# Kernel optimization log

Measured on AMD Instinct MI355X. Metric: run time of the kernel, lower is better.

## Reference

```python
import jax, jax.numpy as jnp
import numpy as np

B, F0, D = 2048, 39, 16
LAYER_SIZES = [128, 128, 128]  # split_half=True -> field_nums [39, 64, 64]


def setup_inputs() -> dict:
    key = jax.random.key(0)
    ks = jax.random.split(key, 1 + 2 * len(LAYER_SIZES))
    inputs = jax.random.normal(ks[0], (B, F0, D), dtype=jnp.float32)
    out = {"inputs": inputs}
    field_nums = [F0]
    for i, size in enumerate(LAYER_SIZES):
        fk = field_nums[-1]
        fan_in = F0 * fk  # conv1d filter fan-in (kernel width 1)
        scale = np.sqrt(2.0 / (fan_in + size)).astype(np.float32)  # glorot
        # filter stored as [F0, Fk, size]; TF flat index is h0*Fk + hk
        out[f"w{i}"] = jax.random.normal(ks[1 + 2 * i], (F0, fk, size), dtype=jnp.float32) * scale
        out[f"b{i}"] = jnp.zeros((size,), dtype=jnp.float32)
        field_nums.append(size // 2)  # split_half=True
    return out


def reference(inputs, w0, w1, w2, b0, b1, b2):
    # CIN: per-embedding-dim outer product of x0 and x_{k-1}, then 1x1 conv
    # (shared dense over field pairs). Fused here as a single einsum per layer.
    x0 = inputs  # [B, F0, D]
    xk = inputs  # [B, Fk, D]
    params = [(w0, b0), (w1, b1), (w2, b2)]
    n_layers = len(params)
    direct = []
    for idx, (W, b) in enumerate(params):
        # out[b, s, d] = sum_{h,k} x0[b,h,d] * xk[b,k,d] * W[h,k,s]
        z = jnp.einsum('bhd,bkd,hks->bsd', x0, xk, W) + b[None, :, None]
        z = jax.nn.relu(z)  # activation='relu'
        if idx != n_layers - 1:
            half = z.shape[1] // 2  # split_half: first half feeds next layer
            xk = z[:, :half, :]
            direct.append(z[:, half:, :])
        else:
            direct.append(z)
    logit = jnp.sum(jnp.concatenate(direct, axis=1), axis=-1)  # [B, 64+64+128]
    return logit
```

## Files before the change

### kernel.cpp

```cpp
#include <hip/hip_runtime.h>
#include <stdint.h>
#include <stddef.h>

#define F0N  39
#define SN   128
#define NB   4
#define X0TS 44
#define XKTS 72
#define WBLK 8192
#define NHB  117

typedef __attribute__((ext_vector_type(8))) short short8;
typedef __attribute__((ext_vector_type(4))) float floatx4;

__device__ __forceinline__ uint16_t f2bf(float f) {
  uint32_t u = __float_as_uint(f);
  u += 0x7fffu + ((u >> 16) & 1u);
  return (uint16_t)(u >> 16);
}

__global__ __launch_bounds__(256) void cin_prepass(
    const float* __restrict__ w0, const float* __restrict__ w1,
    const float* __restrict__ w2, uint16_t* __restrict__ wt) {
  __shared__ float T[64 * 132];
  const int bc = blockIdx.x;
  const int L = bc / F0N;
  const int h = bc - L * F0N;
  const float* W = (L == 0) ? w0 : ((L == 1) ? w1 : w2);
  const int fk = (L == 0) ? 39 : 64;
  const int tid = threadIdx.x;

  for (int e = tid; e < 8192; e += 256) {
    int k = e >> 7, s = e & 127;
    T[k * 132 + s] = (k < fk) ? W[(h * fk + k) * SN + s] : 0.0f;
  }
  __syncthreads();
  uint32_t* dst = (uint32_t*)(wt + (size_t)bc * WBLK);
  for (int i = tid; i < 4096; i += 256) {
    int frag = i >> 8, w = i & 255;
    int st = frag >> 1, ch = frag & 1;
    int ln = w >> 2, jp = w & 3;
    int quad = ln >> 4, l16 = ln & 15;
    int k0 = ch * 32 + quad * 8 + jp * 2;
    int s = st * 16 + l16;
    dst[i] = (uint32_t)f2bf(T[k0 * 132 + s]) | ((uint32_t)f2bf(T[(k0 + 1) * 132 + s]) << 16);
  }
}

__global__ __launch_bounds__(512) void cin_main(
    const float* __restrict__ x,
    const float* __restrict__ bias0, const float* __restrict__ bias1,
    const float* __restrict__ bias2,
    const uint16_t* __restrict__ wt,
    float* __restrict__ out) {

  __shared__ __align__(16) float    X0T[NB * 16 * X0TS];
  __shared__ __align__(16) uint16_t XKT[NB * 16 * XKTS];

  const int tid  = threadIdx.x;
  const int lane = tid & 63;
  const int st   = tid >> 6;
  const int l16  = lane & 15;
  const int quad = lane >> 4;
  const int bbase = blockIdx.x * NB;

  {
    float* p = X0T;
#pragma unroll
    for (int i = 0; i < 6; i++) { int e = tid + 512 * i; if (e < 2816) p[e] = 0.f; }
    uint32_t* q = (uint32_t*)XKT;
#pragma unroll
    for (int i = 0; i < 5; i++) { int e = tid + 512 * i; if (e < 2304) q[e] = 0u; }
  }
  __syncthreads();

#pragma unroll
  for (int it = 0; it < 5; ++it) {
    int e = tid + it * 512;
    if (e < NB * F0N * 16) {
      float v = x[(size_t)bbase * (F0N * 16) + e];
      int d = e & 15, p = e >> 4;
      int b = p / F0N, h = p - b * F0N;
      X0T[(b * 16 + d) * X0TS + h] = v;
    }
  }
  __syncthreads();

  if (tid < 256) {
    int b = tid >> 6, d = (tid >> 2) & 15, kg = tid & 3;
    const float* src = &X0T[(b * 16 + d) * X0TS];
    uint32_t* drow = (uint32_t*)&XKT[(b * 16 + d) * XKTS + kg * 16];
#pragma unroll
    for (int i2 = 0; i2 < 8; i2++) {
      int k0 = kg * 16 + i2 * 2;
      uint32_t lo = (k0 < 39)     ? (uint32_t)f2bf(src[k0])     : 0u;
      uint32_t hi = (k0 + 1 < 39) ? (uint32_t)f2bf(src[k0 + 1]) : 0u;
      drow[i2] = lo | (hi << 16);
    }
  }
  __syncthreads();

  const uint16_t* wlane = wt + st * 1024 + (size_t)lane * 8;

  short8 Wc0 = *(const short8*)(wlane);
  short8 Wc1 = *(const short8*)(wlane + 512);

#pragma unroll 1
  for (int L = 0; L < 3; ++L) {
    short8 Bf0[NB], Bf1[NB];
#pragma unroll
    for (int b = 0; b < NB; ++b) {
      const uint16_t* r = XKT + (b * 16 + l16) * XKTS + quad * 8;
      Bf0[b] = *(const short8*)r;
      Bf1[b] = *(const short8*)(r + 32);
    }
    const float* bp = (L == 0) ? bias0 : ((L == 1) ? bias1 : bias2);
    float bvr[4];
#pragma unroll
    for (int r = 0; r < 4; ++r) bvr[r] = bp[st * 16 + quad * 4 + r];

    floatx4 z[NB] = {};
    const floatx4 zero4 = {0.f, 0.f, 0.f, 0.f};

#pragma unroll 1
    for (int h4 = 0; h4 < 10; ++h4) {
      float4 xv[NB];
#pragma unroll
      for (int b = 0; b < NB; ++b)
        xv[b] = *(const float4*)&X0T[(b * 16 + l16) * X0TS + h4 * 4];

#pragma unroll
      for (int hi = 0; hi < 4; ++hi) {
        const int h = h4 * 4 + hi;
        short8 Wn0, Wn1;
        {
          int Ln = L, hh = h + 1;
          if (hh >= 39) { if (L < 2) { Ln = L + 1; hh = 0; } else hh = 38; }
          const uint16_t* wl = wlane + (size_t)(Ln * F0N + hh) * WBLK;
          Wn0 = *(const short8*)wl;
          Wn1 = *(const short8*)(wl + 512);
        }

#pragma unroll
        for (int b = 0; b < NB; ++b) {
          floatx4 y = __builtin_amdgcn_mfma_f32_16x16x32_bf16(Wc0, Bf0[b], zero4, 0, 0, 0);
          y = __builtin_amdgcn_mfma_f32_16x16x32_bf16(Wc1, Bf1[b], y, 0, 0, 0);
          const float xs = (hi == 0) ? xv[b].x : (hi == 1) ? xv[b].y
                         : (hi == 2) ? xv[b].z : xv[b].w;
#pragma unroll
          for (int r = 0; r < 4; ++r) z[b][r] += xs * y[r];
        }
        Wc0 = Wn0;
        Wc1 = Wn1;
      }
    }

#pragma unroll
    for (int b = 0; b < NB; ++b) {
#pragma unroll
      for (int r = 0; r < 4; ++r) {
        float t = fmaxf(z[b][r] + bvr[r], 0.f);
        if (L < 2 && st < 4)
          XKT[(b * 16 + l16) * XKTS + st * 16 + quad * 4 + r] = f2bf(t);
        float s4 = t;
        s4 += __shfl_xor(s4, 1);
        s4 += __shfl_xor(s4, 2);
        s4 += __shfl_xor(s4, 4);
        s4 += __shfl_xor(s4, 8);
        if (l16 == 0) {
          int s = st * 16 + quad * 4 + r;
          if (L == 2)       out[(size_t)(bbase + b) * 256 + 128 + s] = s4;
          else if (s >= 64) out[(size_t)(bbase + b) * 256 + L * 64 + (s - 64)] = s4;
        }
      }
    }
    if (L < 2) __syncthreads();
  }
}

extern "C" void kernel_launch(void* const* d_in, const int* in_sizes, int n_in,
                              void* d_out, int out_size, void* d_ws, size_t ws_size,
                              hipStream_t stream) {
  (void)in_sizes; (void)n_in; (void)out_size; (void)ws_size;
  const float* x  = (const float*)d_in[0];
  const float* w0 = (const float*)d_in[1];
  const float* b0 = (const float*)d_in[2];
  const float* w1 = (const float*)d_in[3];
  const float* b1 = (const float*)d_in[4];
  const float* w2 = (const float*)d_in[5];
  const float* b2 = (const float*)d_in[6];
  uint16_t* wt    = (uint16_t*)d_ws;

  cin_prepass<<<NHB, 256, 0, stream>>>(w0, w1, w2, wt);
  cin_main<<<512, 512, 0, stream>>>(x, b0, b1, b2, wt, (float*)d_out);
}
```

Measured before the change: 158.0 us.

## Double batch per block to 8 with 1024 threads and split prepass

Each main-kernel block now handles 8 batch rows with 16 waves, two waves per output tile, each covering 4 batch rows. The grid halves to 256 blocks, and each block loads each weight fragment once for twice as many batch rows. The h loop is restructured to a single-step loop with scalar X0 loads. The weight prepass is split into 234 half-blocks with a smaller shared buffer to raise its parallelism. The trade-offs are fewer blocks across the CUs and higher per-block LDS and thread pressure.

```diff
diff --git a/kernel.cpp b/kernel.cpp
--- a/kernel.cpp
+++ b/kernel.cpp
@@ -4,11 +4,11 @@
 
 #define F0N  39
 #define SN   128
-#define NB   4
+#define NB   8
 #define X0TS 44
 #define XKTS 72
 #define WBLK 8192
-#define NHB  117
+#define NHB2 234
 
 typedef __attribute__((ext_vector_type(8))) short short8;
 typedef __attribute__((ext_vector_type(4))) float floatx4;
@@ -22,32 +22,35 @@
 __global__ __launch_bounds__(256) void cin_prepass(
     const float* __restrict__ w0, const float* __restrict__ w1,
     const float* __restrict__ w2, uint16_t* __restrict__ wt) {
-  __shared__ float T[64 * 132];
+  __shared__ float T[32 * 132];
   const int bc = blockIdx.x;
-  const int L = bc / F0N;
-  const int h = bc - L * F0N;
+  const int ch = bc & 1;
+  const int lh = bc >> 1;
+  const int L = lh / F0N;
+  const int h = lh - L * F0N;
   const float* W = (L == 0) ? w0 : ((L == 1) ? w1 : w2);
   const int fk = (L == 0) ? 39 : 64;
   const int tid = threadIdx.x;
 
-  for (int e = tid; e < 8192; e += 256) {
-    int k = e >> 7, s = e & 127;
-    T[k * 132 + s] = (k < fk) ? W[(h * fk + k) * SN + s] : 0.0f;
+  for (int e = tid; e < 4096; e += 256) {
+    int kc = e >> 7, s = e & 127;
+    int k = ch * 32 + kc;
+    T[kc * 132 + s] = (k < fk) ? W[(h * fk + k) * SN + s] : 0.0f;
   }
   __syncthreads();
-  uint32_t* dst = (uint32_t*)(wt + (size_t)bc * WBLK);
-  for (int i = tid; i < 4096; i += 256) {
-    int frag = i >> 8, w = i & 255;
-    int st = frag >> 1, ch = frag & 1;
+  uint32_t* dst = (uint32_t*)(wt + (size_t)lh * WBLK);
+  for (int i = tid; i < 2048; i += 256) {
+    int st = i >> 8, w = i & 255;
     int ln = w >> 2, jp = w & 3;
     int quad = ln >> 4, l16 = ln & 15;
-    int k0 = ch * 32 + quad * 8 + jp * 2;
+    int k0 = quad * 8 + jp * 2;
     int s = st * 16 + l16;
-    dst[i] = (uint32_t)f2bf(T[k0 * 132 + s]) | ((uint32_t)f2bf(T[(k0 + 1) * 132 + s]) << 16);
+    dst[(size_t)(st * 2 + ch) * 256 + w] =
+        (uint32_t)f2bf(T[k0 * 132 + s]) | ((uint32_t)f2bf(T[(k0 + 1) * 132 + s]) << 16);
   }
 }
 
-__global__ __launch_bounds__(512) void cin_main(
+__global__ __launch_bounds__(1024) void cin_main(
     const float* __restrict__ x,
     const float* __restrict__ bias0, const float* __restrict__ bias1,
     const float* __restrict__ bias2,
@@ -59,7 +62,9 @@
 
   const int tid  = threadIdx.x;
   const int lane = tid & 63;
-  const int st   = tid >> 6;
+  const int wave = tid >> 6;
+  const int st   = wave >> 1;
+  const int bg   = wave & 1;
   const int l16  = lane & 15;
   const int quad = lane >> 4;
   const int bbase = blockIdx.x * NB;
@@ -67,16 +72,16 @@
   {
     float* p = X0T;
 #pragma unroll
-    for (int i = 0; i < 6; i++) { int e = tid + 512 * i; if (e < 2816) p[e] = 0.f; }
+    for (int i = 0; i < 6; i++) { int e = tid + 1024 * i; if (e < 5632) p[e] = 0.f; }
     uint32_t* q = (uint32_t*)XKT;
 #pragma unroll
-    for (int i = 0; i < 5; i++) { int e = tid + 512 * i; if (e < 2304) q[e] = 0u; }
+    for (int i = 0; i < 5; i++) { int e = tid + 1024 * i; if (e < 4608) q[e] = 0u; }
   }
   __syncthreads();
 
 #pragma unroll
   for (int it = 0; it < 5; ++it) {
-    int e = tid + it * 512;
+    int e = tid + it * 1024;
     if (e < NB * F0N * 16) {
       float v = x[(size_t)bbase * (F0N * 16) + e];
       int d = e & 15, p = e >> 4;
@@ -86,7 +91,7 @@
   }
   __syncthreads();
 
-  if (tid < 256) {
+  if (tid < 512) {
     int b = tid >> 6, d = (tid >> 2) & 15, kg = tid & 3;
     const float* src = &X0T[(b * 16 + d) * X0TS];
     uint32_t* drow = (uint32_t*)&XKT[(b * 16 + d) * XKTS + kg * 16];
@@ -107,59 +112,54 @@
 
 #pragma unroll 1
   for (int L = 0; L < 3; ++L) {
-    short8 Bf0[NB], Bf1[NB];
+    short8 Bf0[4], Bf1[4];
 #pragma unroll
-    for (int b = 0; b < NB; ++b) {
-      const uint16_t* r = XKT + (b * 16 + l16) * XKTS + quad * 8;
-      Bf0[b] = *(const short8*)r;
-      Bf1[b] = *(const short8*)(r + 32);
+    for (int bi = 0; bi < 4; ++bi) {
+      const uint16_t* r = XKT + ((bg * 4 + bi) * 16 + l16) * XKTS + quad * 8;
+      Bf0[bi] = *(const short8*)r;
+      Bf1[bi] = *(const short8*)(r + 32);
     }
     const float* bp = (L == 0) ? bias0 : ((L == 1) ? bias1 : bias2);
     float bvr[4];
 #pragma unroll
     for (int r = 0; r < 4; ++r) bvr[r] = bp[st * 16 + quad * 4 + r];
 
-    floatx4 z[NB] = {};
+    floatx4 z[4] = {};
     const floatx4 zero4 = {0.f, 0.f, 0.f, 0.f};
 
 #pragma unroll 1
-    for (int h4 = 0; h4 < 10; ++h4) {
-      float4 xv[NB];
+    for (int h = 0; h < 40; ++h) {
+      short8 Wn0, Wn1;
+      {
+        int Ln = L, hh = h + 1;
+        if (hh >= 39) { if (L < 2) { Ln = L + 1; hh = 0; } else hh = 38; }
+        const uint16_t* wl = wlane + (size_t)(Ln * F0N + hh) * WBLK;
+        Wn0 = *(const short8*)wl;
+        Wn1 = *(const short8*)(wl + 512);
+      }
+
+      float xs[4];
 #pragma unroll
-      for (int b = 0; b < NB; ++b)
-        xv[b] = *(const float4*)&X0T[(b * 16 + l16) * X0TS + h4 * 4];
+      for (int bi = 0; bi < 4; ++bi)
+        xs[bi] = X0T[((bg * 4 + bi) * 16 + l16) * X0TS + h];
 
 #pragma unroll
-      for (int hi = 0; hi < 4; ++hi) {
-        const int h = h4 * 4 + hi;
-        short8 Wn0, Wn1;
-        {
-          int Ln = L, hh = h + 1;
-          if (hh >= 39) { if (L < 2) { Ln = L + 1; hh = 0; } else hh = 38; }
-          const uint16_t* wl = wlane + (size_t)(Ln * F0N + hh) * WBLK;
-          Wn0 = *(const short8*)wl;
-          Wn1 = *(const short8*)(wl + 512);
-        }
-
+      for (int bi = 0; bi < 4; ++bi) {
+        floatx4 y = __builtin_amdgcn_mfma_f32_16x16x32_bf16(Wc0, Bf0[bi], zero4, 0, 0, 0);
+        y = __builtin_amdgcn_mfma_f32_16x16x32_bf16(Wc1, Bf1[bi], y, 0, 0, 0);
 #pragma unroll
-        for (int b = 0; b < NB; ++b) {
-          floatx4 y = __builtin_amdgcn_mfma_f32_16x16x32_bf16(Wc0, Bf0[b], zero4, 0, 0, 0);
-          y = __builtin_amdgcn_mfma_f32_16x16x32_bf16(Wc1, Bf1[b], y, 0, 0, 0);
-          const float xs = (hi == 0) ? xv[b].x : (hi == 1) ? xv[b].y
-                         : (hi == 2) ? xv[b].z : xv[b].w;
-#pragma unroll
-          for (int r = 0; r < 4; ++r) z[b][r] += xs * y[r];
-        }
-        Wc0 = Wn0;
-        Wc1 = Wn1;
+        for (int r = 0; r < 4; ++r) z[bi][r] += xs[bi] * y[r];
       }
+      Wc0 = Wn0;
+      Wc1 = Wn1;
     }
 
 #pragma unroll
-    for (int b = 0; b < NB; ++b) {
+    for (int bi = 0; bi < 4; ++bi) {
+      const int b = bg * 4 + bi;
 #pragma unroll
       for (int r = 0; r < 4; ++r) {
-        float t = fmaxf(z[b][r] + bvr[r], 0.f);
+        float t = fmaxf(z[bi][r] + bvr[r], 0.f);
         if (L < 2 && st < 4)
           XKT[(b * 16 + l16) * XKTS + st * 16 + quad * 4 + r] = f2bf(t);
         float s4 = t;
@@ -191,6 +191,6 @@
   const float* b2 = (const float*)d_in[6];
   uint16_t* wt    = (uint16_t*)d_ws;
 
-  cin_prepass<<<NHB, 256, 0, stream>>>(w0, w1, w2, wt);
-  cin_main<<<512, 512, 0, stream>>>(x, b0, b1, b2, wt, (float*)d_out);
+  cin_prepass<<<NHB2, 256, 0, stream>>>(w0, w1, w2, wt);
+  cin_main<<<256, 1024, 0, stream>>>(x, b0, b1, b2, wt, (float*)d_out);
 }
```

New measurement: 135.4 us. -14.3%, faster.
